# Kernel optimization log

Hardware: AMD Instinct MI355X
Metric: run time of the kernel (lower is better)

## Reference

```python
import jax, jax.numpy as jnp
import numpy as np

B, S, D, H, V = 4, 1024, 1024, 16, 1024
HD = D // H  # head_dim = 64
FF = 4 * D


def _layer_norm(x, g, b, eps=1e-5):
    mu = jnp.mean(x, axis=-1, keepdims=True)
    var = jnp.var(x, axis=-1, keepdims=True)
    return (x - mu) * jax.lax.rsqrt(var + eps) * g + b


def _pos_encoding(seq_len, d_model):
    # sinusoidal PE, matching PositionalEncoding buffer construction
    pos = jnp.arange(seq_len, dtype=jnp.float32)[:, None]
    div = jnp.exp(jnp.arange(0, d_model, 2, dtype=jnp.float32) * (-np.log(10000.0) / d_model))
    pe = jnp.zeros((seq_len, d_model), dtype=jnp.float32)
    pe = pe.at[:, 0::2].set(jnp.sin(pos * div))
    pe = pe.at[:, 1::2].set(jnp.cos(pos * div))
    return pe


def setup_inputs() -> dict:
    key = jax.random.key(0)
    ks = jax.random.split(key, 12)
    sc = 0.02
    return {
        "inputs": jax.random.randint(ks[0], (B, S), 0, V, dtype=jnp.int32),
        "targets": jax.random.randint(ks[1], (B, S), 0, V, dtype=jnp.int32),
        "wte": jax.random.normal(ks[2], (V, D), jnp.float32) * sc,
        "wq": jax.random.normal(ks[3], (D, D), jnp.float32) * sc,
        "bq": jnp.zeros((D,), jnp.float32),
        "wk": jax.random.normal(ks[4], (D, D), jnp.float32) * sc,
        "bk": jnp.zeros((D,), jnp.float32),
        "wv": jax.random.normal(ks[5], (D, D), jnp.float32) * sc,
        "bv": jnp.zeros((D,), jnp.float32),
        "wo": jax.random.normal(ks[6], (D, D), jnp.float32) * sc,
        "bo": jnp.zeros((D,), jnp.float32),
        "w1": jax.random.normal(ks[7], (D, FF), jnp.float32) * sc,
        "b1": jnp.zeros((FF,), jnp.float32),
        "w2": jax.random.normal(ks[8], (FF, D), jnp.float32) * sc,
        "b2": jnp.zeros((D,), jnp.float32),
        "ln1_g": jnp.ones((D,), jnp.float32),
        "ln1_b": jnp.zeros((D,), jnp.float32),
        "ln2_g": jnp.ones((D,), jnp.float32),
        "ln2_b": jnp.zeros((D,), jnp.float32),
    }


def reference(inputs, targets, wte, wq, bq, wk, bk, wv, bv, wo, bo,
              w1, b1, w2, b2, ln1_g, ln1_b, ln2_g, ln2_b):
    # embedding + positional encoding
    x = wte[inputs] + _pos_encoding(S, D)  # [B,S,D]

    # naive causal multi-head attention (dropout = identity in eval)
    q = (x @ wq + bq).reshape(B, S, H, HD)
    k = (x @ wk + bk).reshape(B, S, H, HD)
    v = (x @ wv + bv).reshape(B, S, H, HD)
    scores = jnp.einsum('bqhd,bkhd->bhqk', q, k) / np.sqrt(HD)  # [B,H,S,S]
    causal = jnp.tril(jnp.ones((S, S), dtype=bool))
    scores = jnp.where(causal, scores, -jnp.inf)
    attn = jax.nn.softmax(scores, axis=-1)
    ctx = jnp.einsum('bhqk,bkhd->bqhd', attn, v).reshape(B, S, D)
    att_out = ctx @ wo + bo

    # residual + LN1, FFN + GELU, residual + LN2
    adn = _layer_norm(x + att_out, ln1_g, ln1_b)
    h = jax.nn.gelu(adn @ w1 + b1, approximate=False) @ w2 + b2
    logits = _layer_norm(h + adn, ln2_g, ln2_b)

    # cross-entropy over d_model(=vocab) classes
    logits_flat = logits.reshape(B * S, D)
    tgt = targets.reshape(B * S)
    logp = jax.nn.log_softmax(logits_flat, axis=-1)
    loss = -jnp.mean(jnp.take_along_axis(logp, tgt[:, None], axis=-1))
    return logits_flat, loss
```

## Files before the change

### kernel.cpp

```cpp
#include <hip/hip_runtime.h>
#include <math.h>

#define BB 4
#define SS 1024
#define DD 1024
#define HH 16
#define HDIM 64
#define FF 4096
#define MM 4096

typedef short bf16x8 __attribute__((ext_vector_type(8)));
typedef short bf16x4 __attribute__((ext_vector_type(4)));
typedef float f32x4  __attribute__((ext_vector_type(4)));

static __device__ __forceinline__ short f2bf(float f){
  unsigned u = __float_as_uint(f);
  u += 0x7FFFu + ((u >> 16) & 1u);
  return (short)(u >> 16);
}
static __device__ __forceinline__ float b2f(short s){
  return __uint_as_float(((unsigned)(unsigned short)s) << 16);
}

static __device__ __forceinline__ float erf_fast(float x){
  float ax = fabsf(x);
  float t  = __builtin_amdgcn_rcpf(1.0f + 0.3275911f * ax);
  float p  = t * (0.254829592f + t * (-0.284496736f + t * (1.421413741f +
             t * (-1.453152027f + t * 1.061405429f))));
  float e  = 1.0f - p * __expf(-ax * ax);
  return copysignf(e, x);
}

static __device__ __forceinline__ void gl_lds16(const short* g, short* l){
  __builtin_amdgcn_global_load_lds((const __attribute__((address_space(1))) unsigned int*)g,
                                   (__attribute__((address_space(3))) unsigned int*)l,
                                   16, 0, 0);
}

__global__ __launch_bounds__(256) void trans_all_kernel(
    const float* __restrict__ wq, const float* __restrict__ wk,
    const float* __restrict__ wv, const float* __restrict__ wo,
    const float* __restrict__ w1, const float* __restrict__ w2,
    short* __restrict__ wqkvt, short* __restrict__ wot,
    short* __restrict__ w1t,   short* __restrict__ w2t){
  __shared__ float t[32][33];
  int idx = blockIdx.x;
  const float* src; short* dst; int R, C, cx, ry;
  if (idx < 4096){
    int wsel = idx >> 10, tt = idx & 1023;
    cx = tt & 31; ry = tt >> 5; R = 1024; C = 1024;
    src = (wsel == 0) ? wq : (wsel == 1) ? wk : (wsel == 2) ? wv : wo;
    dst = (wsel == 3) ? wot : wqkvt + (size_t)wsel * 1024 * 1024;
  } else if (idx < 8192){
    int tt = idx - 4096; cx = tt & 127; ry = tt >> 7; R = 1024; C = 4096;
    src = w1; dst = w1t;
  } else {
    int tt = idx - 8192; cx = tt & 31; ry = tt >> 5; R = 4096; C = 1024;
    src = w2; dst = w2t;
  }
  int c0 = cx * 32, r0 = ry * 32;
  int tx = threadIdx.x, ty = threadIdx.y;
#pragma unroll
  for (int i = 0; i < 32; i += 8)
    t[ty + i][tx] = src[(size_t)(r0 + ty + i) * C + (c0 + tx)];
  __syncthreads();
#pragma unroll
  for (int i = 0; i < 32; i += 8)
    dst[(size_t)(c0 + ty + i) * R + (r0 + tx)] = f2bf(t[tx][ty + i]);
}

__global__ __launch_bounds__(256) void concat_bias_kernel(const float* __restrict__ a,
                                                          const float* __restrict__ b,
                                                          const float* __restrict__ c,
                                                          float* __restrict__ dst){
  int t = blockIdx.x * 256 + threadIdx.x;
  float v = (t < 1024) ? a[t] : (t < 2048 ? b[t - 1024] : c[t - 2048]);
  dst[t] = v;
}

__global__ __launch_bounds__(256) void embed_kernel(const int* __restrict__ inputs,
                                                    const float* __restrict__ wte,
                                                    short* __restrict__ xb){
  int idx4 = blockIdx.x * 256 + threadIdx.x;
  int row = idx4 >> 8;
  int d   = (idx4 & 255) * 4;
  int s   = row & (SS - 1);
  int tok = inputs[row];
  float4 w = *(const float4*)&wte[(size_t)tok * DD + d];
  const float cdiv = -9.210340371976184f / 512.0f;
  int i0 = d >> 1;
  float ang0 = (float)s * expf((float)i0 * cdiv);
  float ang1 = (float)s * expf((float)(i0 + 1) * cdiv);
  float x0 = w.x + sinf(ang0);
  float x1 = w.y + cosf(ang0);
  float x2 = w.z + sinf(ang1);
  float x3 = w.w + cosf(ang1);
  bf16x4 sb; sb[0]=f2bf(x0); sb[1]=f2bf(x1); sb[2]=f2bf(x2); sb[3]=f2bf(x3);
  *(bf16x4*)&xb[(size_t)row * DD + d] = sb;
}

template<int MODE, bool GELU, bool ADDBIAS>
__global__ __launch_bounds__(256) void gemm128_kernel(const short* __restrict__ A,
    const short* __restrict__ Bt, const float* __restrict__ bias,
    short* __restrict__ o0, short* __restrict__ o1,
    short* __restrict__ o2, short* __restrict__ o3,
    short* __restrict__ qo, short* __restrict__ ko, short* __restrict__ vto,
    int M, int N, int K, int Kc){
  __shared__ __align__(16) short a_lds[3][128 * 32];
  __shared__ __align__(16) short b_lds[3][128 * 32];
  int tid = threadIdx.x;
  int lid = blockIdx.y * gridDim.x + blockIdx.x;
  int cpx = (gridDim.x * gridDim.y) >> 3;
  int swz = (lid & 7) * cpx + (lid >> 3);
  int n0 = (swz % gridDim.x) * 128;
  int m0 = (swz / gridDim.x) * 128;
  int bz = blockIdx.z;
  int kbeg = bz * Kc;
  int w = tid >> 6, lane = tid & 63, lr = lane & 15, lg = lane >> 4;
  int wm = (w & 1) * 64, wn = (w >> 1) * 64;
  int srow = lane >> 2, scol = (lane & 3) * 8;
  f32x4 acc[4][4] = {};

  const short* Arow = A  + (size_t)(m0 + srow) * K + kbeg + scol;
  const short* Brow = Bt + (size_t)(n0 + srow) * K + kbeg + scol;

  auto STAGE = [&](int buf, int k0){
#pragma unroll
    for (int i = 0; i < 2; i++){
      int rb = (w + 4 * i) * 16;
      gl_lds16(Arow + (size_t)rb * K + k0, &a_lds[buf][rb * 32]);
      gl_lds16(Brow + (size_t)rb * K + k0, &b_lds[buf][rb * 32]);
    }
  };

  int nst = Kc >> 5;
  STAGE(0, 0);
  STAGE(1, 32);
  asm volatile("s_waitcnt vmcnt(4)" ::: "memory");
  __builtin_amdgcn_s_barrier();
  __builtin_amdgcn_sched_barrier(0);

  int cur = 0;
  for (int it = 0; it < nst; it++){
    int stg = cur + 2; if (stg >= 3) stg -= 3;
    if (it + 2 < nst) STAGE(stg, (it + 2) << 5);

    bf16x8 af[4], bfr[4];
#pragma unroll
    for (int mi = 0; mi < 4; mi++)
      af[mi] = *(const bf16x8*)&a_lds[cur][(wm + mi * 16 + lr) * 32 + lg * 8];
#pragma unroll
    for (int ni = 0; ni < 4; ni++)
      bfr[ni] = *(const bf16x8*)&b_lds[cur][(wn + ni * 16 + lr) * 32 + lg * 8];
#pragma unroll
    for (int mi = 0; mi < 4; mi++)
#pragma unroll
      for (int ni = 0; ni < 4; ni++)
        acc[mi][ni] = __builtin_amdgcn_mfma_f32_16x16x32_bf16(af[mi], bfr[ni], acc[mi][ni], 0, 0, 0);

    if (it + 2 < nst) asm volatile("s_waitcnt vmcnt(4)" ::: "memory");
    else              asm volatile("s_waitcnt vmcnt(0)" ::: "memory");
    __builtin_amdgcn_s_barrier();
    __builtin_amdgcn_sched_barrier(0);
    cur = cur + 1; if (cur >= 3) cur -= 3;
  }

  short* slab = (MODE == 1) ? ((bz == 0) ? o0 : (bz == 1) ? o1 : (bz == 2) ? o2 : o3) : o0;
  bool addb = ADDBIAS && (MODE != 1 || bz == 0);
#pragma unroll
  for (int mi = 0; mi < 4; mi++){
#pragma unroll
    for (int ni = 0; ni < 4; ni++){
      int ng = n0 + wn + ni * 16 + lr;
      float bv = addb ? bias[ng] : 0.0f;
      int mg0 = m0 + wm + mi * 16 + 4 * lg;
      if (MODE == 2){
        int sel = n0 >> 10;
        if (sel == 2){
          int d = ng & 1023; int hh = d >> 6, nn = d & 63;
          int bI = mg0 >> 10, sI = mg0 & 1023;
          bf16x4 pk;
#pragma unroll
          for (int r = 0; r < 4; r++) pk[r] = f2bf(acc[mi][ni][r] + bv);
          *(bf16x4*)&vto[(((size_t)(bI * HH + hh)) * HDIM + nn) * SS + sI] = pk;
        } else {
          short* dst = (sel == 0) ? qo : ko;
#pragma unroll
          for (int r = 0; r < 4; r++)
            dst[(size_t)(mg0 + r) * DD + (ng & 1023)] = f2bf(acc[mi][ni][r] + bv);
        }
      } else {
#pragma unroll
        for (int r = 0; r < 4; r++){
          float v = acc[mi][ni][r] + bv;
          if (GELU) v = 0.5f * v * (1.0f + erf_fast(v * 0.70710678118654752f));
          slab[(size_t)(mg0 + r) * N + ng] = f2bf(v);
        }
      }
    }
  }
}

__global__ __launch_bounds__(256) void attn_kernel(const short* __restrict__ qb,
                                                   const short* __restrict__ kb,
                                                   const short* __restrict__ vtb,
                                                   short* __restrict__ ctxb){
  __shared__ __align__(16) short k_lds[2][64 * 64];
  __shared__ __align__(16) short v_lds[2][64 * 64];
  __shared__ __align__(16) short p_lds[4][2][16 * 72];
  int qp = blockIdx.x, h = blockIdx.y, b = blockIdx.z;
  int Tlo = qp, Thi = 15 - qp;
  int tid = threadIdx.x, w = tid >> 6, lane = tid & 63, lr = lane & 15, lg = lane >> 4;

  const short* kp0 = kb  + (size_t)b * SS * DD + h * HDIM;
  const short* vt0 = vtb + (size_t)(b * HH + h) * HDIM * SS;

  bf16x8 qf0[2], qf1[2];
#pragma unroll
  for (int ti = 0; ti < 2; ti++){
    int T = ti ? Thi : Tlo;
    const short* qp_ = qb + ((size_t)(b * SS + T * 64 + w * 16 + lr) * DD + h * HDIM);
    qf0[ti] = *(const bf16x8*)&qp_[lg * 8];
    qf1[ti] = *(const bf16x8*)&qp_[32 + lg * 8];
  }

  float m[2][4], l[2][4];
  f32x4 acc[2][4] = {};
#pragma unroll
  for (int ti = 0; ti < 2; ti++)
#pragma unroll
    for (int r = 0; r < 4; r++){ m[ti][r] = -1e30f; l[ti][r] = 0.0f; }

  int srow8 = lane >> 3;
  int sjs   = (lane & 7) ^ srow8;
  auto STAGE = [&](int buf, int kt){
#pragma unroll
    for (int i = 0; i < 2; i++){
      int rb  = (w + 4 * i) * 8;
      int row = rb + srow8;
      gl_lds16(kp0 + (size_t)(kt * 64 + row) * DD + sjs * 8, &k_lds[buf][rb * 64]);
      gl_lds16(vt0 + (size_t)row * SS + kt * 64 + sjs * 8,   &v_lds[buf][rb * 64]);
    }
  };

  int cur = 0;
  STAGE(0, 0);
  asm volatile("s_waitcnt vmcnt(0)" ::: "memory");
  __syncthreads();

  bf16x8 pf0[2], pf1[2];
  for (int kt = 0; kt <= Thi; kt++){
    if (kt < Thi) STAGE(cur ^ 1, kt + 1);

    bf16x8 kf0[4], kf1[4];
#pragma unroll
    for (int sub = 0; sub < 4; sub++){
      int r = sub * 16 + lr;
      kf0[sub] = *(const bf16x8*)&k_lds[cur][r * 64 + ((lg     ^ (r & 7)) * 8)];
      kf1[sub] = *(const bf16x8*)&k_lds[cur][r * 64 + (((lg+4) ^ (r & 7)) * 8)];
    }

#pragma unroll
    for (int ti = 0; ti < 2; ti++){
      int T = ti ? Thi : Tlo;
      if (kt > T) continue;
      f32x4 sc4[4];
#pragma unroll
      for (int sub = 0; sub < 4; sub++){
        f32x4 t = {};
        t = __builtin_amdgcn_mfma_f32_16x16x32_bf16(qf0[ti], kf0[sub], t, 0, 0, 0);
        t = __builtin_amdgcn_mfma_f32_16x16x32_bf16(qf1[ti], kf1[sub], t, 0, 0, 0);
#pragma unroll
        for (int r = 0; r < 4; r++) t[r] *= 0.125f;
        sc4[sub] = t;
      }
      if (kt == T){
#pragma unroll
        for (int sub = 0; sub < 4; sub++)
#pragma unroll
          for (int r = 0; r < 4; r++)
            if (16 * sub + lr > 16 * w + 4 * lg + r) sc4[sub][r] = -1e30f;
      }

      float pm[4];
#pragma unroll
      for (int r = 0; r < 4; r++)
        pm[r] = fmaxf(fmaxf(sc4[0][r], sc4[1][r]), fmaxf(sc4[2][r], sc4[3][r]));
#pragma unroll
      for (int off = 1; off < 16; off <<= 1)
#pragma unroll
        for (int r = 0; r < 4; r++) pm[r] = fmaxf(pm[r], __shfl_xor(pm[r], off));

      float scl[4], rs[4];
#pragma unroll
      for (int r = 0; r < 4; r++){
        float mn = fmaxf(m[ti][r], pm[r]);
        scl[r] = __expf(m[ti][r] - mn);
        m[ti][r] = mn;
        rs[r] = 0.0f;
      }
#pragma unroll
      for (int sub = 0; sub < 4; sub++)
#pragma unroll
        for (int r = 0; r < 4; r++){
          float p = __expf(sc4[sub][r] - m[ti][r]);
          sc4[sub][r] = p;
          rs[r] += p;
        }
#pragma unroll
      for (int off = 1; off < 16; off <<= 1)
#pragma unroll
        for (int r = 0; r < 4; r++) rs[r] += __shfl_xor(rs[r], off);
#pragma unroll
      for (int r = 0; r < 4; r++) l[ti][r] = l[ti][r] * scl[r] + rs[r];
#pragma unroll
      for (int nb = 0; nb < 4; nb++)
#pragma unroll
        for (int r = 0; r < 4; r++) acc[ti][nb][r] *= scl[r];

      short* pw = &p_lds[w][ti][0];
#pragma unroll
      for (int sub = 0; sub < 4; sub++)
#pragma unroll
        for (int r = 0; r < 4; r++)
          pw[(4 * lg + r) * 72 + sub * 16 + lr] = f2bf(sc4[sub][r]);
      pf0[ti] = *(const bf16x8*)&pw[lr * 72 + lg * 8];
      pf1[ti] = *(const bf16x8*)&pw[lr * 72 + 32 + lg * 8];
    }

    bf16x8 vf0[4], vf1[4];
#pragma unroll
    for (int nb = 0; nb < 4; nb++){
      int r = nb * 16 + lr;
      vf0[nb] = *(const bf16x8*)&v_lds[cur][r * 64 + ((lg     ^ (r & 7)) * 8)];
      vf1[nb] = *(const bf16x8*)&v_lds[cur][r * 64 + (((lg+4) ^ (r & 7)) * 8)];
    }

#pragma unroll
    for (int ti = 0; ti < 2; ti++){
      int T = ti ? Thi : Tlo;
      if (kt > T) continue;
#pragma unroll
      for (int nb = 0; nb < 4; nb++){
        acc[ti][nb] = __builtin_amdgcn_mfma_f32_16x16x32_bf16(pf0[ti], vf0[nb], acc[ti][nb], 0, 0, 0);
        acc[ti][nb] = __builtin_amdgcn_mfma_f32_16x16x32_bf16(pf1[ti], vf1[nb], acc[ti][nb], 0, 0, 0);
      }
    }

    asm volatile("s_waitcnt vmcnt(0)" ::: "memory");
    __syncthreads();
    cur ^= 1;
  }

#pragma unroll
  for (int ti = 0; ti < 2; ti++){
    int T = ti ? Thi : Tlo;
#pragma unroll
    for (int r = 0; r < 4; r++){
      float inv = 1.0f / l[ti][r];
      int row = T * 64 + w * 16 + 4 * lg + r;
#pragma unroll
      for (int nb = 0; nb < 4; nb++)
        ctxb[(size_t)(b * SS + row) * DD + h * HDIM + nb * 16 + lr] = f2bf(acc[ti][nb][r] * inv);
    }
  }
}

template<int NPART, bool WF32, bool LOSS>
__global__ __launch_bounds__(256) void ln_kernel(const short* __restrict__ p0,
                                                 const short* __restrict__ p1,
                                                 const short* __restrict__ p2,
                                                 const short* __restrict__ p3,
                                                 const short* __restrict__ resb,
                                                 const float* __restrict__ g,
                                                 const float* __restrict__ be,
                                                 float* __restrict__ of,
                                                 short* __restrict__ ob,
                                                 const int* __restrict__ tgt,
                                                 float* __restrict__ lrow){
  int row = blockIdx.x, tid = threadIdx.x;
  size_t base = (size_t)row * DD + tid * 4;
  bf16x4 rv = *(const bf16x4*)&resb[base];
  float x0 = b2f(rv[0]), x1 = b2f(rv[1]), x2 = b2f(rv[2]), x3 = b2f(rv[3]);
  const short* ps[4] = {p0, p1, p2, p3};
#pragma unroll
  for (int p = 0; p < NPART; p++){
    bf16x4 pv = *(const bf16x4*)&ps[p][base];
    x0 += b2f(pv[0]); x1 += b2f(pv[1]); x2 += b2f(pv[2]); x3 += b2f(pv[3]);
  }
  float s = x0 + x1 + x2 + x3;
  float q = x0 * x0 + x1 * x1 + x2 * x2 + x3 * x3;
#pragma unroll
  for (int off = 32; off; off >>= 1){ s += __shfl_xor(s, off); q += __shfl_xor(q, off); }
  __shared__ float red[9];
  if ((tid & 63) == 0){ red[tid >> 6] = s; red[4 + (tid >> 6)] = q; }
  __syncthreads();
  s = red[0] + red[1] + red[2] + red[3];
  q = red[4] + red[5] + red[6] + red[7];
  float mean = s * (1.0f / DD);
  float var  = q * (1.0f / DD) - mean * mean;
  float rstd = rsqrtf(var + 1e-5f);
  float4 gv  = *(const float4*)&g[tid * 4];
  float4 bev = *(const float4*)&be[tid * 4];
  float y0 = (x0 - mean) * rstd * gv.x + bev.x;
  float y1 = (x1 - mean) * rstd * gv.y + bev.y;
  float y2 = (x2 - mean) * rstd * gv.z + bev.z;
  float y3 = (x3 - mean) * rstd * gv.w + bev.w;
  if (WF32){
    *(float4*)&of[base] = make_float4(y0, y1, y2, y3);
  } else {
    bf16x4 sb; sb[0]=f2bf(y0); sb[1]=f2bf(y1); sb[2]=f2bf(y2); sb[3]=f2bf(y3);
    *(bf16x4*)&ob[base] = sb;
  }
  if (LOSS){
    __syncthreads();
    float mx = fmaxf(fmaxf(y0, y1), fmaxf(y2, y3));
#pragma unroll
    for (int off = 32; off; off >>= 1) mx = fmaxf(mx, __shfl_xor(mx, off));
    if ((tid & 63) == 0) red[tid >> 6] = mx;
    int t = tgt[row];
    if (tid == (t >> 2))
      red[8] = ((t & 3) == 0) ? y0 : ((t & 3) == 1) ? y1 : ((t & 3) == 2) ? y2 : y3;
    __syncthreads();
    mx = fmaxf(fmaxf(red[0], red[1]), fmaxf(red[2], red[3]));
    float se = __expf(y0 - mx) + __expf(y1 - mx) + __expf(y2 - mx) + __expf(y3 - mx);
#pragma unroll
    for (int off = 32; off; off >>= 1) se += __shfl_xor(se, off);
    if ((tid & 63) == 0) red[4 + (tid >> 6)] = se;
    __syncthreads();
    if (tid == 0){
      float tot = red[4] + red[5] + red[6] + red[7];
      lrow[row] = mx + logf(tot) - red[8];
    }
  }
}

__global__ __launch_bounds__(256) void loss_reduce_kernel(const float* __restrict__ pr,
                                                          float* __restrict__ outp){
  int tid = threadIdx.x;
  float s = 0.0f;
  for (int i = tid; i < MM; i += 256) s += pr[i];
#pragma unroll
  for (int off = 32; off; off >>= 1) s += __shfl_xor(s, off);
  __shared__ float red[4];
  if ((tid & 63) == 0) red[tid >> 6] = s;
  __syncthreads();
  if (tid == 0) outp[0] = (red[0] + red[1] + red[2] + red[3]) * (1.0f / MM);
}

extern "C" void kernel_launch(void* const* d_in, const int* in_sizes, int n_in,
                              void* d_out, int out_size, void* d_ws, size_t ws_size,
                              hipStream_t stream){
  const int*   inputs  = (const int*)  d_in[0];
  const int*   targets = (const int*)  d_in[1];
  const float* wte     = (const float*)d_in[2];
  const float* wq      = (const float*)d_in[3];
  const float* bq      = (const float*)d_in[4];
  const float* wk      = (const float*)d_in[5];
  const float* bk      = (const float*)d_in[6];
  const float* wv      = (const float*)d_in[7];
  const float* bvv     = (const float*)d_in[8];
  const float* wo      = (const float*)d_in[9];
  const float* bo      = (const float*)d_in[10];
  const float* w1      = (const float*)d_in[11];
  const float* b1      = (const float*)d_in[12];
  const float* w2      = (const float*)d_in[13];
  const float* b2      = (const float*)d_in[14];
  const float* ln1g    = (const float*)d_in[15];
  const float* ln1b    = (const float*)d_in[16];
  const float* ln2g    = (const float*)d_in[17];
  const float* ln2b    = (const float*)d_in[18];
  float* out = (float*)d_out;

  char* ws = (char*)d_ws;
  const size_t MB = 1024 * 1024;
  short* wqkvt = (short*)(ws + 0 * MB);
  short* wot   = (short*)(ws + 6 * MB);
  short* w1t   = (short*)(ws + 8 * MB);
  short* w2t   = (short*)(ws + 16 * MB);
  short* xb    = (short*)(ws + 24 * MB);
  short* qbuf  = (short*)(ws + 32 * MB);
  short* kbuf  = (short*)(ws + 40 * MB);
  short* vtb   = (short*)(ws + 48 * MB);
  short* ctxb  = (short*)(ws + 56 * MB);
  short* pr0   = (short*)(ws + 64 * MB);
  short* pr1   = (short*)(ws + 72 * MB);
  short* adnb  = (short*)(ws + 80 * MB);
  short* h1b   = (short*)(ws + 32 * MB);
  short* hs0   = (short*)(ws + 64 * MB);
  short* hs1   = (short*)(ws + 72 * MB);
  short* hs2   = (short*)(ws + 88 * MB);
  short* hs3   = (short*)(ws + 96 * MB);
  float* lrow  = (float*)(ws + 104 * MB);
  float* bqkv  = (float*)(ws + 105 * MB);

  trans_all_kernel<<<12288, dim3(32, 8), 0, stream>>>(
      wq, wk, wv, wo, w1, w2, wqkvt, wot, w1t, w2t);
  concat_bias_kernel<<<12, 256, 0, stream>>>(bq, bk, bvv, bqkv);

  embed_kernel<<<4096, 256, 0, stream>>>(inputs, wte, xb);

  gemm128_kernel<2, false, true><<<dim3(24, 32), 256, 0, stream>>>(
      xb, wqkvt, bqkv, nullptr, nullptr, nullptr, nullptr,
      qbuf, kbuf, vtb, MM, 3 * DD, DD, DD);

  attn_kernel<<<dim3(8, 16, 4), 256, 0, stream>>>(qbuf, kbuf, vtb, ctxb);

  gemm128_kernel<1, false, true><<<dim3(8, 32, 2), 256, 0, stream>>>(
      ctxb, wot, bo, pr0, pr1, nullptr, nullptr,
      nullptr, nullptr, nullptr, MM, DD, DD, 512);

  ln_kernel<2, false, false><<<4096, 256, 0, stream>>>(
      pr0, pr1, nullptr, nullptr, xb, ln1g, ln1b, nullptr, adnb, nullptr, nullptr);

  gemm128_kernel<0, true, true><<<dim3(32, 32), 256, 0, stream>>>(
      adnb, w1t, b1, h1b, nullptr, nullptr, nullptr,
      nullptr, nullptr, nullptr, MM, FF, DD, DD);

  gemm128_kernel<1, false, true><<<dim3(8, 32, 4), 256, 0, stream>>>(
      h1b, w2t, b2, hs0, hs1, hs2, hs3,
      nullptr, nullptr, nullptr, MM, DD, FF, 1024);

  ln_kernel<4, true, true><<<4096, 256, 0, stream>>>(
      hs0, hs1, hs2, hs3, adnb, ln2g, ln2b, out, nullptr, targets, lrow);

  loss_reduce_kernel<<<1, 256, 0, stream>>>(lrow, out + (size_t)MM * DD);
}
```

Before: 258.6 us.

## Use 256x256 GEMM tiles with 512 threads, 4-stage pipeline and swizzled LDS

Replaces the 128x128, 256-thread GEMM with a 256x256 tile computed by 8 waves, each owning a 128x64 sub-tile. The software pipeline grows from 3 to 4 LDS stages, with XOR-swizzled LDS layout to avoid bank conflicts and s_setprio around the MFMA block. The output-projection GEMM moves from split-K 2 to split-K 4, so LN1 now reduces four partial slabs and workspace offsets are reshuffled. The larger tiles raise data reuse per block, but use about 128KB of LDS and launch only 192–256 blocks, which limits occupancy and may leave CUs idle.

```diff
diff --git a/kernel.cpp b/kernel.cpp
--- a/kernel.cpp
+++ b/kernel.cpp
@@ -100,80 +100,87 @@
 }
 
 template<int MODE, bool GELU, bool ADDBIAS>
-__global__ __launch_bounds__(256) void gemm128_kernel(const short* __restrict__ A,
+__global__ __launch_bounds__(512) void gemm256_kernel(const short* __restrict__ A,
     const short* __restrict__ Bt, const float* __restrict__ bias,
     short* __restrict__ o0, short* __restrict__ o1,
     short* __restrict__ o2, short* __restrict__ o3,
     short* __restrict__ qo, short* __restrict__ ko, short* __restrict__ vto,
     int M, int N, int K, int Kc){
-  __shared__ __align__(16) short a_lds[3][128 * 32];
-  __shared__ __align__(16) short b_lds[3][128 * 32];
+  __shared__ __align__(16) short lds[4][2][8192];
   int tid = threadIdx.x;
   int lid = blockIdx.y * gridDim.x + blockIdx.x;
   int cpx = (gridDim.x * gridDim.y) >> 3;
   int swz = (lid & 7) * cpx + (lid >> 3);
-  int n0 = (swz % gridDim.x) * 128;
-  int m0 = (swz / gridDim.x) * 128;
+  int n0 = (swz % gridDim.x) * 256;
+  int m0 = (swz / gridDim.x) * 256;
   int bz = blockIdx.z;
   int kbeg = bz * Kc;
   int w = tid >> 6, lane = tid & 63, lr = lane & 15, lg = lane >> 4;
-  int wm = (w & 1) * 64, wn = (w >> 1) * 64;
-  int srow = lane >> 2, scol = (lane & 3) * 8;
-  f32x4 acc[4][4] = {};
-
+  int wm = w >> 2, wn = w & 3;
+  f32x4 acc[8][4] = {};
+
+  int srow = w * 16 + (lane >> 2);
+  int scol = (((lane & 3) ^ ((lane >> 3) & 3)) * 8);
   const short* Arow = A  + (size_t)(m0 + srow) * K + kbeg + scol;
   const short* Brow = Bt + (size_t)(n0 + srow) * K + kbeg + scol;
 
-  auto STAGE = [&](int buf, int k0){
-#pragma unroll
-    for (int i = 0; i < 2; i++){
-      int rb = (w + 4 * i) * 16;
-      gl_lds16(Arow + (size_t)rb * K + k0, &a_lds[buf][rb * 32]);
-      gl_lds16(Brow + (size_t)rb * K + k0, &b_lds[buf][rb * 32]);
+  auto STAGE = [&](int buf, int kt){
+    int k0 = kt * 32;
+#pragma unroll
+    for (int j = 0; j < 2; j++){
+      gl_lds16(Arow + (size_t)(j * 128) * K + k0, &lds[buf][0][j * 4096 + w * 512]);
+      gl_lds16(Brow + (size_t)(j * 128) * K + k0, &lds[buf][1][j * 4096 + w * 512]);
     }
   };
 
   int nst = Kc >> 5;
   STAGE(0, 0);
-  STAGE(1, 32);
-  asm volatile("s_waitcnt vmcnt(4)" ::: "memory");
-  __builtin_amdgcn_s_barrier();
-  __builtin_amdgcn_sched_barrier(0);
-
-  int cur = 0;
+  if (nst > 1) STAGE(1, 1);
+  if (nst > 2) STAGE(2, 2);
+
+  int axor = ((lr >> 1) & 3) << 4;
+
   for (int it = 0; it < nst; it++){
-    int stg = cur + 2; if (stg >= 3) stg -= 3;
-    if (it + 2 < nst) STAGE(stg, (it + 2) << 5);
-
-    bf16x8 af[4], bfr[4];
-#pragma unroll
-    for (int mi = 0; mi < 4; mi++)
-      af[mi] = *(const bf16x8*)&a_lds[cur][(wm + mi * 16 + lr) * 32 + lg * 8];
-#pragma unroll
-    for (int ni = 0; ni < 4; ni++)
-      bfr[ni] = *(const bf16x8*)&b_lds[cur][(wn + ni * 16 + lr) * 32 + lg * 8];
-#pragma unroll
-    for (int mi = 0; mi < 4; mi++)
+    if (it + 3 < nst) STAGE((it + 3) & 3, it + 3);
+    if (it + 3 < nst)      asm volatile("s_waitcnt vmcnt(12)" ::: "memory");
+    else if (it + 2 < nst) asm volatile("s_waitcnt vmcnt(8)"  ::: "memory");
+    else if (it + 1 < nst) asm volatile("s_waitcnt vmcnt(4)"  ::: "memory");
+    else                   asm volatile("s_waitcnt vmcnt(0)"  ::: "memory");
+    __builtin_amdgcn_s_barrier();
+
+    const short* la = &lds[it & 3][0][0];
+    const short* lb = &lds[it & 3][1][0];
+    bf16x8 bfrag[4], afrag[8];
+#pragma unroll
+    for (int ni = 0; ni < 4; ni++){
+      int off = ((((wn * 64 + ni * 16 + lr) * 64) + lg * 16) ^ axor) >> 1;
+      bfrag[ni] = *(const bf16x8*)&lb[off];
+    }
+#pragma unroll
+    for (int mi = 0; mi < 8; mi++){
+      int off = ((((wm * 128 + mi * 16 + lr) * 64) + lg * 16) ^ axor) >> 1;
+      afrag[mi] = *(const bf16x8*)&la[off];
+    }
+    __builtin_amdgcn_s_setprio(1);
+#pragma unroll
+    for (int mi = 0; mi < 8; mi++)
 #pragma unroll
       for (int ni = 0; ni < 4; ni++)
-        acc[mi][ni] = __builtin_amdgcn_mfma_f32_16x16x32_bf16(af[mi], bfr[ni], acc[mi][ni], 0, 0, 0);
-
-    if (it + 2 < nst) asm volatile("s_waitcnt vmcnt(4)" ::: "memory");
-    else              asm volatile("s_waitcnt vmcnt(0)" ::: "memory");
+        acc[mi][ni] = __builtin_amdgcn_mfma_f32_16x16x32_bf16(afrag[mi], bfrag[ni], acc[mi][ni], 0, 0, 0);
+    __builtin_amdgcn_s_setprio(0);
+    asm volatile("" ::: "memory");
     __builtin_amdgcn_s_barrier();
-    __builtin_amdgcn_sched_barrier(0);
-    cur = cur + 1; if (cur >= 3) cur -= 3;
   }
 
   short* slab = (MODE == 1) ? ((bz == 0) ? o0 : (bz == 1) ? o1 : (bz == 2) ? o2 : o3) : o0;
   bool addb = ADDBIAS && (MODE != 1 || bz == 0);
 #pragma unroll
-  for (int mi = 0; mi < 4; mi++){
+  for (int mi = 0; mi < 8; mi++){
 #pragma unroll
     for (int ni = 0; ni < 4; ni++){
-      int ng = n0 + wn + ni * 16 + lr;
+      int ng = n0 + wn * 64 + ni * 16 + lr;
       float bv = addb ? bias[ng] : 0.0f;
-      int mg0 = m0 + wm + mi * 16 + 4 * lg;
+      int mg0 = m0 + wm * 128 + mi * 16 + 4 * lg;
       if (MODE == 2){
         int sel = n0 >> 10;
         if (sel == 2){
@@ -485,12 +492,14 @@
   short* ctxb  = (short*)(ws + 56 * MB);
   short* pr0   = (short*)(ws + 64 * MB);
   short* pr1   = (short*)(ws + 72 * MB);
-  short* adnb  = (short*)(ws + 80 * MB);
+  short* pr2   = (short*)(ws + 80 * MB);
+  short* pr3   = (short*)(ws + 88 * MB);
+  short* adnb  = (short*)(ws + 96 * MB);
   short* h1b   = (short*)(ws + 32 * MB);
   short* hs0   = (short*)(ws + 64 * MB);
   short* hs1   = (short*)(ws + 72 * MB);
-  short* hs2   = (short*)(ws + 88 * MB);
-  short* hs3   = (short*)(ws + 96 * MB);
+  short* hs2   = (short*)(ws + 80 * MB);
+  short* hs3   = (short*)(ws + 88 * MB);
   float* lrow  = (float*)(ws + 104 * MB);
   float* bqkv  = (float*)(ws + 105 * MB);
 
@@ -500,24 +509,24 @@
 
   embed_kernel<<<4096, 256, 0, stream>>>(inputs, wte, xb);
 
-  gemm128_kernel<2, false, true><<<dim3(24, 32), 256, 0, stream>>>(
+  gemm256_kernel<2, false, true><<<dim3(12, 16), 512, 0, stream>>>(
       xb, wqkvt, bqkv, nullptr, nullptr, nullptr, nullptr,
       qbuf, kbuf, vtb, MM, 3 * DD, DD, DD);
 
   attn_kernel<<<dim3(8, 16, 4), 256, 0, stream>>>(qbuf, kbuf, vtb, ctxb);
 
-  gemm128_kernel<1, false, true><<<dim3(8, 32, 2), 256, 0, stream>>>(
-      ctxb, wot, bo, pr0, pr1, nullptr, nullptr,
-      nullptr, nullptr, nullptr, MM, DD, DD, 512);
-
-  ln_kernel<2, false, false><<<4096, 256, 0, stream>>>(
-      pr0, pr1, nullptr, nullptr, xb, ln1g, ln1b, nullptr, adnb, nullptr, nullptr);
-
-  gemm128_kernel<0, true, true><<<dim3(32, 32), 256, 0, stream>>>(
+  gemm256_kernel<1, false, true><<<dim3(4, 16, 4), 512, 0, stream>>>(
+      ctxb, wot, bo, pr0, pr1, pr2, pr3,
+      nullptr, nullptr, nullptr, MM, DD, DD, 256);
+
+  ln_kernel<4, false, false><<<4096, 256, 0, stream>>>(
+      pr0, pr1, pr2, pr3, xb, ln1g, ln1b, nullptr, adnb, nullptr, nullptr);
+
+  gemm256_kernel<0, true, true><<<dim3(16, 16), 512, 0, stream>>>(
       adnb, w1t, b1, h1b, nullptr, nullptr, nullptr,
       nullptr, nullptr, nullptr, MM, FF, DD, DD);
 
-  gemm128_kernel<1, false, true><<<dim3(8, 32, 4), 256, 0, stream>>>(
+  gemm256_kernel<1, false, true><<<dim3(4, 16, 4), 512, 0, stream>>>(
       h1b, w2t, b2, hs0, hs1, hs2, hs3,
       nullptr, nullptr, nullptr, MM, DD, FF, 1024);
 
```

Result: faster. 237.1 us (-8.3%).
